# Kernel optimization log

Hardware: AMD Instinct MI355X
Metric: run time of the kernel (lower is better)

The kernel has to match this reference:

```python
import jax, jax.numpy as jnp
import numpy as np

B, S, H, NH = 2, 2048, 1024, 16
HD = H // NH  # 64
BASE = 10000.0


def _rope_tables(seq_len, head_dim):
    inv_freq = 1.0 / (BASE ** (jnp.arange(0, head_dim, 2, dtype=jnp.float32) / head_dim))
    t = jnp.arange(seq_len, dtype=jnp.float32)
    freqs = jnp.outer(t, inv_freq)            # [S, HD/2]
    emb = jnp.concatenate([freqs, freqs], -1)  # [S, HD]
    return jnp.cos(emb), jnp.sin(emb)


def _rotate_half(x):
    x1, x2 = jnp.split(x, 2, axis=-1)
    return jnp.concatenate([-x2, x1], axis=-1)


def setup_inputs() -> dict:
    key = jax.random.key(0)
    ks = jax.random.split(key, 5)
    sc = 1.0 / np.sqrt(H)
    return {
        "hidden_states": jax.random.normal(ks[0], (B, S, H), jnp.float32),
        "Wq": jax.random.normal(ks[1], (H, H), jnp.float32) * sc,
        "Wk": jax.random.normal(ks[2], (H, H), jnp.float32) * sc,
        "Wv": jax.random.normal(ks[3], (H, H), jnp.float32) * sc,
        "Wo": jax.random.normal(ks[4], (H, H), jnp.float32) * sc,
    }


def reference(hidden_states, Wq, Wk, Wv, Wo):
    b, s, h = hidden_states.shape
    # nn.Linear: y = x @ W.T
    q = hidden_states @ Wq.T
    k = hidden_states @ Wk.T
    v = hidden_states @ Wv.T
    # [B, NH, S, HD]
    q = q.reshape(b, s, NH, HD).transpose(0, 2, 1, 3)
    k = k.reshape(b, s, NH, HD).transpose(0, 2, 1, 3)
    v = v.reshape(b, s, NH, HD).transpose(0, 2, 1, 3)
    cos, sin = _rope_tables(s, HD)  # [S, HD], broadcast over B, NH
    q = q * cos + _rotate_half(q) * sin
    k = k * cos + _rotate_half(k) * sin
    scores = jnp.einsum('bhqd,bhkd->bhqk', q, k) / jnp.sqrt(jnp.float32(HD))
    probs = jax.nn.softmax(scores, axis=-1)
    ctx = jnp.einsum('bhqk,bhkd->bhqd', probs, v)
    ctx = ctx.transpose(0, 2, 1, 3).reshape(b, s, h)
    return ctx @ Wo.T
```

## Files before the change

kernel.cpp:

```cpp
#include <hip/hip_runtime.h>
#include <hip/hip_bf16.h>
#include <math.h>

typedef __hip_bfloat16 bf16;
typedef float f32x4 __attribute__((ext_vector_type(4)));
typedef short s16x8 __attribute__((ext_vector_type(8)));

#define NB 2
#define SEQ 2048
#define HID 1024
#define NHEAD 16
#define HD 64
#define BH (NB * NHEAD)
#define MROWS (NB * SEQ)
#define QSCL 0.18033688011111793f

static __device__ __forceinline__ f32x4 mfma16(s16x8 a, s16x8 b, f32x4 c) {
  return __builtin_amdgcn_mfma_f32_16x16x32_bf16(a, b, c, 0, 0, 0);
}

static __device__ __forceinline__ void gload_lds16(const bf16* g, bf16* l) {
  __builtin_amdgcn_global_load_lds((const __attribute__((address_space(1))) void*)g,
                                   (__attribute__((address_space(3))) void*)l, 16, 0, 0);
}

static __device__ __forceinline__ unsigned pack_bf16(float a, float b) {
  __hip_bfloat162 t = __float22bfloat162_rn(float2{a, b});
  return *(unsigned*)&t;
}

__global__ __launch_bounds__(256) void f2b_kernel(const float* __restrict__ src,
                                                  bf16* __restrict__ dst, int n) {
  int i = (blockIdx.x * 256 + threadIdx.x) * 4;
  if (i >= n) return;
  float4 v = *(const float4*)(src + i);
  bf16 a0 = __float2bfloat16(v.x), a1 = __float2bfloat16(v.y);
  bf16 a2 = __float2bfloat16(v.z), a3 = __float2bfloat16(v.w);
  ushort4 u;
  u.x = *(const unsigned short*)&a0;
  u.y = *(const unsigned short*)&a1;
  u.z = *(const unsigned short*)&a2;
  u.w = *(const unsigned short*)&a3;
  *(ushort4*)(dst + i) = u;
}

__global__ __launch_bounds__(256) void w4b_kernel(const float* __restrict__ wq, const float* __restrict__ wk,
                                                  const float* __restrict__ wv, const float* __restrict__ wo,
                                                  bf16* __restrict__ wqkv, bf16* __restrict__ wob) {
  int wsel = blockIdx.y;
  const float* src = (wsel == 0) ? wq : (wsel == 1) ? wk : (wsel == 2) ? wv : wo;
  bf16* dst = (wsel < 3) ? (wqkv + (size_t)wsel * HID * HID) : wob;
  int i = (blockIdx.x * 256 + threadIdx.x) * 4;
  float4 v = *(const float4*)(src + i);
  bf16 a0 = __float2bfloat16(v.x), a1 = __float2bfloat16(v.y);
  bf16 a2 = __float2bfloat16(v.z), a3 = __float2bfloat16(v.w);
  ushort4 u;
  u.x = *(const unsigned short*)&a0;
  u.y = *(const unsigned short*)&a1;
  u.z = *(const unsigned short*)&a2;
  u.w = *(const unsigned short*)&a3;
  *(ushort4*)(dst + i) = u;
}

__global__ __launch_bounds__(256) void rope_tab_kernel(float* __restrict__ ct, float* __restrict__ st) {
  int i = blockIdx.x * 256 + threadIdx.x;
  int s = i >> 5, j = i & 31;
  float inv = expf(-(float)(2 * j) * (9.210340371976184f / 64.0f));
  float ang = (float)s * inv;
  float sn, cs;
  sincosf(ang, &sn, &cs);
  ct[i] = cs;
  st[i] = sn;
}

template <int MODE>
__global__ __launch_bounds__(256) void gemm_bt(const bf16* __restrict__ A, const bf16* __restrict__ Bm,
                                               float* __restrict__ C,
                                               bf16* __restrict__ Qb, bf16* __restrict__ Kb,
                                               bf16* __restrict__ Vtg,
                                               const float* __restrict__ ct, const float* __restrict__ st,
                                               int M, int N, int K) {
  __shared__ __align__(16) bf16 As[128][32];
  __shared__ __align__(16) bf16 Bs[128][32];
  const int tid = threadIdx.x, lane = tid & 63, wid = tid >> 6;
  const int wm = wid >> 1, wn = wid & 1;
  const int tm = blockIdx.y * 128, tn = blockIdx.x * 128;
  const int lrow = lane >> 2;
  const int lcol = (lane & 3) * 8;

  f32x4 acc[4][4];
#pragma unroll
  for (int i = 0; i < 4; ++i)
#pragma unroll
    for (int j = 0; j < 4; ++j) acc[i][j] = (f32x4){0.f, 0.f, 0.f, 0.f};

  for (int k0 = 0; k0 < K; k0 += 32) {
    __syncthreads();
    {
      int r0 = wid * 32;
      gload_lds16(A  + (size_t)(tm + r0 +      lrow) * K + k0 + lcol, &As[r0][0]);
      gload_lds16(A  + (size_t)(tm + r0 + 16 + lrow) * K + k0 + lcol, &As[r0 + 16][0]);
      gload_lds16(Bm + (size_t)(tn + r0 +      lrow) * K + k0 + lcol, &Bs[r0][0]);
      gload_lds16(Bm + (size_t)(tn + r0 + 16 + lrow) * K + k0 + lcol, &Bs[r0 + 16][0]);
    }
    __syncthreads();
    s16x8 af[4], bfr[4];
#pragma unroll
    for (int mi = 0; mi < 4; ++mi)
      af[mi] = *(const s16x8*)&As[wm * 64 + mi * 16 + (lane & 15)][(lane >> 4) * 8];
#pragma unroll
    for (int ni = 0; ni < 4; ++ni)
      bfr[ni] = *(const s16x8*)&Bs[wn * 64 + ni * 16 + (lane & 15)][(lane >> 4) * 8];
#pragma unroll
    for (int mi = 0; mi < 4; ++mi)
#pragma unroll
      for (int ni = 0; ni < 4; ++ni)
        acc[mi][ni] = mfma16(af[mi], bfr[ni], acc[mi][ni]);
  }

  if (MODE == 0) {
    const int tblk = tn >> 10;
    if (tblk < 2) {
      const float scl = (tblk == 0) ? QSCL : 1.0f;
#pragma unroll
      for (int mi = 0; mi < 4; ++mi) {
#pragma unroll
        for (int r = 0; r < 4; ++r) {
          int row = tm + wm * 64 + mi * 16 + (lane >> 4) * 4 + r;
          int s = row & (SEQ - 1);
#pragma unroll
          for (int p = 0; p < 2; ++p) {
            int j = p * 16 + (lane & 15);
            float c = ct[s * 32 + j], sn = st[s * 32 + j];
            float x0 = acc[mi][p][r], x1 = acc[mi][p + 2][r];
            acc[mi][p][r]     = (x0 * c - x1 * sn) * scl;
            acc[mi][p + 2][r] = (x1 * c + x0 * sn) * scl;
          }
        }
      }
    }
  }

#pragma unroll
  for (int mi = 0; mi < 4; ++mi) {
#pragma unroll
    for (int ni = 0; ni < 4; ++ni) {
#pragma unroll
      for (int r = 0; r < 4; ++r) {
        int row = tm + wm * 64 + mi * 16 + (lane >> 4) * 4 + r;
        int col = tn + wn * 64 + ni * 16 + (lane & 15);
        float v = acc[mi][ni][r];
        if (MODE == 0) {
          int t = col >> 10, c = col & (HID - 1);
          int h = c >> 6, d = c & 63;
          int b = row >> 11, s = row & (SEQ - 1);
          size_t bh = (size_t)(b * NHEAD + h);
          if (t == 0)      Qb[(bh * SEQ + s) * HD + d]  = __float2bfloat16(v);
          else if (t == 1) Kb[(bh * SEQ + s) * HD + d]  = __float2bfloat16(v);
          else             Vtg[(bh * HD + d) * SEQ + s] = __float2bfloat16(v);
        } else {
          C[(size_t)row * N + col] = v;
        }
      }
    }
  }
}

__global__ __launch_bounds__(256) void attn_kernel(const bf16* __restrict__ Q, const bf16* __restrict__ K,
                                                   const bf16* __restrict__ Vt, bf16* __restrict__ ctx) {
  __shared__ __align__(16) bf16 S[8192 + 8192];
  bf16* Ks = S;
  bf16* Vs = S + 8192;
  const int tid = threadIdx.x, l = tid & 63, w = tid >> 6;
  const int g = l >> 4, lq = l & 15;
  const int qb = blockIdx.x, bh = blockIdx.y;

  const bf16* Qp  = Q  + ((size_t)bh * SEQ + qb * 64) * HD;
  const bf16* Kp0 = K  + (size_t)bh * SEQ * HD;
  const bf16* Vp0 = Vt + (size_t)bh * HD * SEQ;

  s16x8 qf[2];
#pragma unroll
  for (int ks = 0; ks < 2; ++ks)
    qf[ks] = *(const s16x8*)(Qp + (w * 16 + lq) * HD + ks * 32 + g * 8);

#pragma unroll
  for (int it = 0; it < 2; ++it) {
    int cb = (it * 4 + w) * 64;
    int R = (cb + l) >> 3;
    int sc = ((l & 7) ^ (R & 7)) * 8;
    int pr = ((R & 32) >> 5) * 32 + ((R & 12) >> 2) * 8 + ((R & 16) >> 4) * 4 + (R & 3);
    gload_lds16(Kp0 + (size_t)pr * HD + sc, Ks + cb * 8);
    gload_lds16(Vp0 + (size_t)R * SEQ + sc, Vs + cb * 8);
  }
  __syncthreads();

  float m_run = -INFINITY, lsum = 0.f;
  f32x4 acc[4];
#pragma unroll
  for (int nf = 0; nf < 4; ++nf) acc[nf] = (f32x4){0.f, 0.f, 0.f, 0.f};

  const int NT = SEQ / 64;
  for (int kvt = 0; kvt < NT; ++kvt) {
    const int cur = kvt & 1;
    if (kvt + 1 < NT) {
      const bf16* Kp = Kp0 + (size_t)(kvt + 1) * 64 * HD;
      const bf16* Vp = Vp0 + (kvt + 1) * 64;
      bf16* Kd = Ks + (1 - cur) * 4096;
      bf16* Vd = Vs + (1 - cur) * 4096;
#pragma unroll
      for (int it = 0; it < 2; ++it) {
        int cb = (it * 4 + w) * 64;
        int R = (cb + l) >> 3;
        int sc = ((l & 7) ^ (R & 7)) * 8;
        int pr = ((R & 32) >> 5) * 32 + ((R & 12) >> 2) * 8 + ((R & 16) >> 4) * 4 + (R & 3);
        gload_lds16(Kp + (size_t)pr * HD + sc, Kd + cb * 8);
        gload_lds16(Vp + (size_t)R * SEQ + sc, Vd + cb * 8);
      }
    }
    const bf16* Kc = Ks + cur * 4096;
    const bf16* Vc = Vs + cur * 4096;

    f32x4 sf[4];
    __builtin_amdgcn_s_setprio(1);
#pragma unroll
    for (int nf = 0; nf < 4; ++nf) {
      f32x4 s = (f32x4){0.f, 0.f, 0.f, 0.f};
      int row = nf * 16 + lq;
#pragma unroll
      for (int ks = 0; ks < 2; ++ks) {
        int slot = (ks * 4 + g) ^ (row & 7);
        s16x8 kf = *(const s16x8*)(Kc + row * 64 + slot * 8);
        s = mfma16(kf, qf[ks], s);
      }
      sf[nf] = s;
    }
    __builtin_amdgcn_s_setprio(0);

    float pmax = sf[0][0];
#pragma unroll
    for (int nf = 0; nf < 4; ++nf)
#pragma unroll
      for (int r = 0; r < 4; ++r) pmax = fmaxf(pmax, sf[nf][r]);
    pmax = fmaxf(pmax, __shfl_xor(pmax, 16));
    pmax = fmaxf(pmax, __shfl_xor(pmax, 32));

    if (__any(pmax > m_run + 8.f)) {
      float mn = fmaxf(m_run, pmax);
      float corr = __builtin_amdgcn_exp2f(m_run - mn);
      m_run = mn;
      lsum *= corr;
      float cq[4];
#pragma unroll
      for (int r = 0; r < 4; ++r) cq[r] = __shfl(corr, g * 4 + r);
#pragma unroll
      for (int nf = 0; nf < 4; ++nf)
#pragma unroll
        for (int r = 0; r < 4; ++r) acc[nf][r] *= cq[r];
    }

    float ls = 0.f;
#pragma unroll
    for (int nf = 0; nf < 4; ++nf)
#pragma unroll
      for (int r = 0; r < 4; ++r) {
        sf[nf][r] = __builtin_amdgcn_exp2f(sf[nf][r] - m_run);
        ls += sf[nf][r];
      }
    lsum += ls;

    s16x8 pf[2];
    {
      unsigned pw[8];
#pragma unroll
      for (int nf = 0; nf < 4; ++nf) {
        pw[nf * 2 + 0] = pack_bf16(sf[nf][0], sf[nf][1]);
        pw[nf * 2 + 1] = pack_bf16(sf[nf][2], sf[nf][3]);
      }
      union { unsigned u[4]; s16x8 v; } c0, c1;
#pragma unroll
      for (int j = 0; j < 4; ++j) { c0.u[j] = pw[j]; c1.u[j] = pw[4 + j]; }
      pf[0] = c0.v;
      pf[1] = c1.v;
    }

    __builtin_amdgcn_s_setprio(1);
#pragma unroll
    for (int nf = 0; nf < 4; ++nf) {
      int row = nf * 16 + lq;
#pragma unroll
      for (int ks = 0; ks < 2; ++ks) {
        int slot = (ks * 4 + g) ^ (row & 7);
        s16x8 vf = *(const s16x8*)(Vc + row * 64 + slot * 8);
        acc[nf] = mfma16(pf[ks], vf, acc[nf]);
      }
    }
    __builtin_amdgcn_s_setprio(0);
    __syncthreads();
  }

  lsum += __shfl_xor(lsum, 16);
  lsum += __shfl_xor(lsum, 32);
  float lr[4];
#pragma unroll
  for (int r = 0; r < 4; ++r) lr[r] = __shfl(lsum, g * 4 + r);

  int b = bh >> 4, h = bh & (NHEAD - 1);
#pragma unroll
  for (int nf = 0; nf < 4; ++nf) {
#pragma unroll
    for (int r = 0; r < 4; ++r) {
      int s = qb * 64 + w * 16 + g * 4 + r;
      int d = nf * 16 + lq;
      float o = acc[nf][r] / lr[r];
      ctx[((size_t)b * SEQ + s) * HID + h * HD + d] = __float2bfloat16(o);
    }
  }
}

extern "C" void kernel_launch(void* const* d_in, const int* in_sizes, int n_in,
                              void* d_out, int out_size, void* d_ws, size_t ws_size,
                              hipStream_t stream) {
  const float* X  = (const float*)d_in[0];
  const float* Wq = (const float*)d_in[1];
  const float* Wk = (const float*)d_in[2];
  const float* Wv = (const float*)d_in[3];
  const float* Wo = (const float*)d_in[4];

  char* p = (char*)d_ws;
  bf16* Xb   = (bf16*)p; p += (size_t)MROWS * HID * 2;
  bf16* Wqkv = (bf16*)p; p += (size_t)3 * HID * HID * 2;
  bf16* Wob  = (bf16*)p; p += (size_t)HID * HID * 2;
  bf16* Qb   = (bf16*)p; p += (size_t)BH * SEQ * HD * 2;
  bf16* Kb   = (bf16*)p; p += (size_t)BH * SEQ * HD * 2;
  bf16* Vtg  = (bf16*)p; p += (size_t)BH * HD * SEQ * 2;
  bf16* Cb   = (bf16*)p; p += (size_t)MROWS * HID * 2;
  float* ct  = (float*)p; p += (size_t)SEQ * 32 * 4;
  float* st  = (float*)p; p += (size_t)SEQ * 32 * 4;

  f2b_kernel<<<(MROWS * HID) / 1024, 256, 0, stream>>>(X, Xb, MROWS * HID);
  w4b_kernel<<<dim3((HID * HID) / 1024, 4), 256, 0, stream>>>(Wq, Wk, Wv, Wo, Wqkv, Wob);
  rope_tab_kernel<<<(SEQ * 32) / 256, 256, 0, stream>>>(ct, st);

  gemm_bt<0><<<dim3(3 * HID / 128, MROWS / 128), 256, 0, stream>>>(
      Xb, Wqkv, nullptr, Qb, Kb, Vtg, ct, st, MROWS, 3 * HID, HID);

  attn_kernel<<<dim3(SEQ / 64, BH), 256, 0, stream>>>(Qb, Kb, Vtg, Cb);

  gemm_bt<1><<<dim3(HID / 128, MROWS / 128), 256, 0, stream>>>(
      Cb, Wob, (float*)d_out, nullptr, nullptr, nullptr, nullptr, nullptr, MROWS, HID, HID);
}
```

Before: 153.5 us.

## Use 32x32 MFMA attention with 128-row query tiles and fuse prep kernels

The attention kernel moves from 16x16x32 to 32x32x16 bf16 MFMA tiles. Each block now covers 128 query rows instead of 64 (each wave handles 32), so every staged K/V tile is reused across twice as many queries and per-iteration overhead is amortised. A remapped 1D grid groups blocks of the same head across XCDs, and the three preprocessing kernels (input cast, weight cast, rope table) are merged into one launch. The costs are higher register pressure from the 16-wide accumulators and half as many blocks (512), which lowers parallelism.

```diff
diff --git a/kernel.cpp b/kernel.cpp
--- a/kernel.cpp
+++ b/kernel.cpp
@@ -4,6 +4,7 @@
 
 typedef __hip_bfloat16 bf16;
 typedef float f32x4 __attribute__((ext_vector_type(4)));
+typedef float f32x16 __attribute__((ext_vector_type(16)));
 typedef short s16x8 __attribute__((ext_vector_type(8)));
 
 #define NB 2
@@ -18,6 +19,9 @@
 static __device__ __forceinline__ f32x4 mfma16(s16x8 a, s16x8 b, f32x4 c) {
   return __builtin_amdgcn_mfma_f32_16x16x32_bf16(a, b, c, 0, 0, 0);
 }
+static __device__ __forceinline__ f32x16 mfma32(s16x8 a, s16x8 b, f32x16 c) {
+  return __builtin_amdgcn_mfma_f32_32x32x16_bf16(a, b, c, 0, 0, 0);
+}
 
 static __device__ __forceinline__ void gload_lds16(const bf16* g, bf16* l) {
   __builtin_amdgcn_global_load_lds((const __attribute__((address_space(1))) void*)g,
@@ -29,48 +33,45 @@
   return *(unsigned*)&t;
 }
 
-__global__ __launch_bounds__(256) void f2b_kernel(const float* __restrict__ src,
-                                                  bf16* __restrict__ dst, int n) {
-  int i = (blockIdx.x * 256 + threadIdx.x) * 4;
-  if (i >= n) return;
-  float4 v = *(const float4*)(src + i);
-  bf16 a0 = __float2bfloat16(v.x), a1 = __float2bfloat16(v.y);
-  bf16 a2 = __float2bfloat16(v.z), a3 = __float2bfloat16(v.w);
-  ushort4 u;
-  u.x = *(const unsigned short*)&a0;
-  u.y = *(const unsigned short*)&a1;
-  u.z = *(const unsigned short*)&a2;
-  u.w = *(const unsigned short*)&a3;
-  *(ushort4*)(dst + i) = u;
-}
-
-__global__ __launch_bounds__(256) void w4b_kernel(const float* __restrict__ wq, const float* __restrict__ wk,
-                                                  const float* __restrict__ wv, const float* __restrict__ wo,
-                                                  bf16* __restrict__ wqkv, bf16* __restrict__ wob) {
-  int wsel = blockIdx.y;
-  const float* src = (wsel == 0) ? wq : (wsel == 1) ? wk : (wsel == 2) ? wv : wo;
-  bf16* dst = (wsel < 3) ? (wqkv + (size_t)wsel * HID * HID) : wob;
-  int i = (blockIdx.x * 256 + threadIdx.x) * 4;
-  float4 v = *(const float4*)(src + i);
-  bf16 a0 = __float2bfloat16(v.x), a1 = __float2bfloat16(v.y);
-  bf16 a2 = __float2bfloat16(v.z), a3 = __float2bfloat16(v.w);
-  ushort4 u;
-  u.x = *(const unsigned short*)&a0;
-  u.y = *(const unsigned short*)&a1;
-  u.z = *(const unsigned short*)&a2;
-  u.w = *(const unsigned short*)&a3;
-  *(ushort4*)(dst + i) = u;
-}
-
-__global__ __launch_bounds__(256) void rope_tab_kernel(float* __restrict__ ct, float* __restrict__ st) {
-  int i = blockIdx.x * 256 + threadIdx.x;
-  int s = i >> 5, j = i & 31;
-  float inv = expf(-(float)(2 * j) * (9.210340371976184f / 64.0f));
-  float ang = (float)s * inv;
-  float sn, cs;
-  sincosf(ang, &sn, &cs);
-  ct[i] = cs;
-  st[i] = sn;
+__global__ __launch_bounds__(256) void prep_kernel(const float* __restrict__ X,
+                                                   const float* __restrict__ wq, const float* __restrict__ wk,
+                                                   const float* __restrict__ wv, const float* __restrict__ wo,
+                                                   bf16* __restrict__ Xb, bf16* __restrict__ wqkv,
+                                                   bf16* __restrict__ wob,
+                                                   float* __restrict__ ct, float* __restrict__ st) {
+  int bid = blockIdx.x, tid = threadIdx.x;
+  if (bid < 8192) {
+    const float* src;
+    bf16* dst;
+    int i;
+    if (bid < 4096) {
+      src = X; dst = Xb;
+      i = (bid * 256 + tid) * 4;
+    } else {
+      int wsel = (bid - 4096) >> 10;
+      src = (wsel == 0) ? wq : (wsel == 1) ? wk : (wsel == 2) ? wv : wo;
+      dst = (wsel < 3) ? (wqkv + (size_t)wsel * HID * HID) : wob;
+      i = (((bid - 4096) & 1023) * 256 + tid) * 4;
+    }
+    float4 v = *(const float4*)(src + i);
+    bf16 a0 = __float2bfloat16(v.x), a1 = __float2bfloat16(v.y);
+    bf16 a2 = __float2bfloat16(v.z), a3 = __float2bfloat16(v.w);
+    ushort4 u;
+    u.x = *(const unsigned short*)&a0;
+    u.y = *(const unsigned short*)&a1;
+    u.z = *(const unsigned short*)&a2;
+    u.w = *(const unsigned short*)&a3;
+    *(ushort4*)(dst + i) = u;
+  } else {
+    int i = (bid - 8192) * 256 + tid;
+    int s = i >> 5, j = i & 31;
+    float inv = expf(-(float)(2 * j) * (9.210340371976184f / 64.0f));
+    float ang = (float)s * inv;
+    float sn, cs;
+    sincosf(ang, &sn, &cs);
+    ct[i] = cs;
+    st[i] = sn;
+  }
 }
 
 template <int MODE>
@@ -168,81 +169,74 @@
 
 __global__ __launch_bounds__(256) void attn_kernel(const bf16* __restrict__ Q, const bf16* __restrict__ K,
                                                    const bf16* __restrict__ Vt, bf16* __restrict__ ctx) {
-  __shared__ __align__(16) bf16 S[8192 + 8192];
+  __shared__ __align__(16) bf16 S[16384];
   bf16* Ks = S;
   bf16* Vs = S + 8192;
   const int tid = threadIdx.x, l = tid & 63, w = tid >> 6;
-  const int g = l >> 4, lq = l & 15;
-  const int qb = blockIdx.x, bh = blockIdx.y;
-
-  const bf16* Qp  = Q  + ((size_t)bh * SEQ + qb * 64) * HD;
+  const int lq = l & 31, hi = l >> 5;
+
+  const int id = blockIdx.x;
+  const int lin = (id & 7) * 64 + (id >> 3);
+  const int bh = lin >> 4, qb = lin & 15;
+
+  const bf16* Qp  = Q  + ((size_t)bh * SEQ + qb * 128) * HD;
   const bf16* Kp0 = K  + (size_t)bh * SEQ * HD;
   const bf16* Vp0 = Vt + (size_t)bh * HD * SEQ;
 
-  s16x8 qf[2];
-#pragma unroll
-  for (int ks = 0; ks < 2; ++ks)
-    qf[ks] = *(const s16x8*)(Qp + (w * 16 + lq) * HD + ks * 32 + g * 8);
-
-#pragma unroll
-  for (int it = 0; it < 2; ++it) {
-    int cb = (it * 4 + w) * 64;
-    int R = (cb + l) >> 3;
-    int sc = ((l & 7) ^ (R & 7)) * 8;
-    int pr = ((R & 32) >> 5) * 32 + ((R & 12) >> 2) * 8 + ((R & 16) >> 4) * 4 + (R & 3);
-    gload_lds16(Kp0 + (size_t)pr * HD + sc, Ks + cb * 8);
-    gload_lds16(Vp0 + (size_t)R * SEQ + sc, Vs + cb * 8);
-  }
+  s16x8 qf[4];
+  {
+    const bf16* qr = Qp + (w * 32 + lq) * HD + hi * 8;
+#pragma unroll
+    for (int ks = 0; ks < 4; ++ks) qf[ks] = *(const s16x8*)(qr + ks * 16);
+  }
+
+  const int s0 = tid, s1 = tid + 256;
+  const int R0 = s0 >> 3, R1 = s1 >> 3;
+  const int c0 = ((s0 & 7) ^ (R0 & 7)) * 8;
+  const int c1 = ((s1 & 7) ^ (R1 & 7)) * 8;
+  const int p0 = (R0 & 51) | ((R0 & 4) << 1) | ((R0 & 8) >> 1);
+  const int p1 = (R1 & 51) | ((R1 & 4) << 1) | ((R1 & 8) >> 1);
+  const bf16* kS0 = Kp0 + p0 * HD + c0;
+  const bf16* kS1 = Kp0 + p1 * HD + c1;
+  const bf16* vS0 = Vp0 + (size_t)R0 * SEQ + c0;
+  const bf16* vS1 = Vp0 + (size_t)R1 * SEQ + c1;
+
+#define STAGE(t, b)                                        \
+  do {                                                     \
+    gload_lds16(kS0 + (t) * (64 * HD), Ks + (b) * 4096 + s0 * 8); \
+    gload_lds16(kS1 + (t) * (64 * HD), Ks + (b) * 4096 + s1 * 8); \
+    gload_lds16(vS0 + (t) * 64,        Vs + (b) * 4096 + s0 * 8); \
+    gload_lds16(vS1 + (t) * 64,        Vs + (b) * 4096 + s1 * 8); \
+  } while (0)
+
+  STAGE(0, 0);
   __syncthreads();
 
   float m_run = -INFINITY, lsum = 0.f;
-  f32x4 acc[4];
-#pragma unroll
-  for (int nf = 0; nf < 4; ++nf) acc[nf] = (f32x4){0.f, 0.f, 0.f, 0.f};
+  f32x16 acc0{}, acc1{};
 
   const int NT = SEQ / 64;
   for (int kvt = 0; kvt < NT; ++kvt) {
     const int cur = kvt & 1;
-    if (kvt + 1 < NT) {
-      const bf16* Kp = Kp0 + (size_t)(kvt + 1) * 64 * HD;
-      const bf16* Vp = Vp0 + (kvt + 1) * 64;
-      bf16* Kd = Ks + (1 - cur) * 4096;
-      bf16* Vd = Vs + (1 - cur) * 4096;
-#pragma unroll
-      for (int it = 0; it < 2; ++it) {
-        int cb = (it * 4 + w) * 64;
-        int R = (cb + l) >> 3;
-        int sc = ((l & 7) ^ (R & 7)) * 8;
-        int pr = ((R & 32) >> 5) * 32 + ((R & 12) >> 2) * 8 + ((R & 16) >> 4) * 4 + (R & 3);
-        gload_lds16(Kp + (size_t)pr * HD + sc, Kd + cb * 8);
-        gload_lds16(Vp + (size_t)R * SEQ + sc, Vd + cb * 8);
-      }
-    }
+    if (kvt + 1 < NT) STAGE(kvt + 1, cur ^ 1);
     const bf16* Kc = Ks + cur * 4096;
     const bf16* Vc = Vs + cur * 4096;
 
-    f32x4 sf[4];
+    f32x16 sf0{}, sf1{};
     __builtin_amdgcn_s_setprio(1);
 #pragma unroll
-    for (int nf = 0; nf < 4; ++nf) {
-      f32x4 s = (f32x4){0.f, 0.f, 0.f, 0.f};
-      int row = nf * 16 + lq;
-#pragma unroll
-      for (int ks = 0; ks < 2; ++ks) {
-        int slot = (ks * 4 + g) ^ (row & 7);
-        s16x8 kf = *(const s16x8*)(Kc + row * 64 + slot * 8);
-        s = mfma16(kf, qf[ks], s);
-      }
-      sf[nf] = s;
+    for (int ks = 0; ks < 4; ++ks) {
+      const int slot = (ks * 2 + hi) ^ (lq & 7);
+      sf0 = mfma32(*(const s16x8*)(Kc + lq * 64 + slot * 8),        qf[ks], sf0);
+      sf1 = mfma32(*(const s16x8*)(Kc + (32 + lq) * 64 + slot * 8), qf[ks], sf1);
     }
     __builtin_amdgcn_s_setprio(0);
 
-    float pmax = sf[0][0];
-#pragma unroll
-    for (int nf = 0; nf < 4; ++nf)
-#pragma unroll
-      for (int r = 0; r < 4; ++r) pmax = fmaxf(pmax, sf[nf][r]);
-    pmax = fmaxf(pmax, __shfl_xor(pmax, 16));
+    float pmax = sf0[0];
+#pragma unroll
+    for (int i = 1; i < 16; ++i) pmax = fmaxf(pmax, sf0[i]);
+#pragma unroll
+    for (int i = 0; i < 16; ++i) pmax = fmaxf(pmax, sf1[i]);
     pmax = fmaxf(pmax, __shfl_xor(pmax, 32));
 
     if (__any(pmax > m_run + 8.f)) {
@@ -250,71 +244,60 @@
       float corr = __builtin_amdgcn_exp2f(m_run - mn);
       m_run = mn;
       lsum *= corr;
-      float cq[4];
-#pragma unroll
-      for (int r = 0; r < 4; ++r) cq[r] = __shfl(corr, g * 4 + r);
-#pragma unroll
-      for (int nf = 0; nf < 4; ++nf)
-#pragma unroll
-        for (int r = 0; r < 4; ++r) acc[nf][r] *= cq[r];
+#pragma unroll
+      for (int r = 0; r < 16; ++r) {
+        float cr = __shfl(corr, (r & 3) + 8 * (r >> 2) + 4 * hi);
+        acc0[r] *= cr;
+        acc1[r] *= cr;
+      }
     }
 
     float ls = 0.f;
 #pragma unroll
-    for (int nf = 0; nf < 4; ++nf)
-#pragma unroll
-      for (int r = 0; r < 4; ++r) {
-        sf[nf][r] = __builtin_amdgcn_exp2f(sf[nf][r] - m_run);
-        ls += sf[nf][r];
+    for (int i = 0; i < 16; ++i) {
+      sf0[i] = __builtin_amdgcn_exp2f(sf0[i] - m_run);
+      ls += sf0[i];
+    }
+#pragma unroll
+    for (int i = 0; i < 16; ++i) {
+      sf1[i] = __builtin_amdgcn_exp2f(sf1[i] - m_run);
+      ls += sf1[i];
+    }
+    lsum += ls;
+
+    s16x8 pf[4];
+#pragma unroll
+    for (int kt = 0; kt < 4; ++kt) {
+      union { unsigned u[4]; s16x8 v; } cc;
+#pragma unroll
+      for (int vv = 0; vv < 4; ++vv) {
+        if (kt < 2) cc.u[vv] = pack_bf16(sf0[(kt & 1) * 8 + 2 * vv], sf0[(kt & 1) * 8 + 2 * vv + 1]);
+        else        cc.u[vv] = pack_bf16(sf1[(kt & 1) * 8 + 2 * vv], sf1[(kt & 1) * 8 + 2 * vv + 1]);
       }
-    lsum += ls;
-
-    s16x8 pf[2];
-    {
-      unsigned pw[8];
-#pragma unroll
-      for (int nf = 0; nf < 4; ++nf) {
-        pw[nf * 2 + 0] = pack_bf16(sf[nf][0], sf[nf][1]);
-        pw[nf * 2 + 1] = pack_bf16(sf[nf][2], sf[nf][3]);
-      }
-      union { unsigned u[4]; s16x8 v; } c0, c1;
-#pragma unroll
-      for (int j = 0; j < 4; ++j) { c0.u[j] = pw[j]; c1.u[j] = pw[4 + j]; }
-      pf[0] = c0.v;
-      pf[1] = c1.v;
+      pf[kt] = cc.v;
     }
 
     __builtin_amdgcn_s_setprio(1);
 #pragma unroll
-    for (int nf = 0; nf < 4; ++nf) {
-      int row = nf * 16 + lq;
-#pragma unroll
-      for (int ks = 0; ks < 2; ++ks) {
-        int slot = (ks * 4 + g) ^ (row & 7);
-        s16x8 vf = *(const s16x8*)(Vc + row * 64 + slot * 8);
-        acc[nf] = mfma16(pf[ks], vf, acc[nf]);
-      }
+    for (int kt = 0; kt < 4; ++kt) {
+      const int slot = (kt * 2 + hi) ^ (lq & 7);
+      acc0 = mfma32(pf[kt], *(const s16x8*)(Vc + lq * 64 + slot * 8),        acc0);
+      acc1 = mfma32(pf[kt], *(const s16x8*)(Vc + (32 + lq) * 64 + slot * 8), acc1);
     }
     __builtin_amdgcn_s_setprio(0);
     __syncthreads();
   }
-
-  lsum += __shfl_xor(lsum, 16);
+#undef STAGE
+
   lsum += __shfl_xor(lsum, 32);
-  float lr[4];
-#pragma unroll
-  for (int r = 0; r < 4; ++r) lr[r] = __shfl(lsum, g * 4 + r);
-
-  int b = bh >> 4, h = bh & (NHEAD - 1);
-#pragma unroll
-  for (int nf = 0; nf < 4; ++nf) {
-#pragma unroll
-    for (int r = 0; r < 4; ++r) {
-      int s = qb * 64 + w * 16 + g * 4 + r;
-      int d = nf * 16 + lq;
-      float o = acc[nf][r] / lr[r];
-      ctx[((size_t)b * SEQ + s) * HID + h * HD + d] = __float2bfloat16(o);
-    }
+  const int b = bh >> 4, h = bh & (NHEAD - 1);
+#pragma unroll
+  for (int r = 0; r < 16; ++r) {
+    int q = (r & 3) + 8 * (r >> 2) + 4 * hi;
+    float inv = 1.0f / __shfl(lsum, q);
+    size_t base = ((size_t)b * SEQ + qb * 128 + w * 32 + q) * HID + h * HD + lq;
+    ctx[base]      = __float2bfloat16(acc0[r] * inv);
+    ctx[base + 32] = __float2bfloat16(acc1[r] * inv);
   }
 }
 
@@ -338,14 +321,12 @@
   float* ct  = (float*)p; p += (size_t)SEQ * 32 * 4;
   float* st  = (float*)p; p += (size_t)SEQ * 32 * 4;
 
-  f2b_kernel<<<(MROWS * HID) / 1024, 256, 0, stream>>>(X, Xb, MROWS * HID);
-  w4b_kernel<<<dim3((HID * HID) / 1024, 4), 256, 0, stream>>>(Wq, Wk, Wv, Wo, Wqkv, Wob);
-  rope_tab_kernel<<<(SEQ * 32) / 256, 256, 0, stream>>>(ct, st);
+  prep_kernel<<<8448, 256, 0, stream>>>(X, Wq, Wk, Wv, Wo, Xb, Wqkv, Wob, ct, st);
 
   gemm_bt<0><<<dim3(3 * HID / 128, MROWS / 128), 256, 0, stream>>>(
       Xb, Wqkv, nullptr, Qb, Kb, Vtg, ct, st, MROWS, 3 * HID, HID);
 
-  attn_kernel<<<dim3(SEQ / 64, BH), 256, 0, stream>>>(Qb, Kb, Vtg, Cb);
+  attn_kernel<<<dim3(512), 256, 0, stream>>>(Qb, Kb, Vtg, Cb);
 
   gemm_bt<1><<<dim3(HID / 128, MROWS / 128), 256, 0, stream>>>(
       Cb, Wob, (float*)d_out, nullptr, nullptr, nullptr, nullptr, nullptr, MROWS, HID, HID);
```

Result: faster. 140.7 us (-8.4%).
